# Kernel tuning notes

Measured on AMD Instinct MI355X. Metric: run time of the kernel, lower is better.

Reference implementation:

```python
import jax, jax.numpy as jnp
import numpy as np
import math

B, S, D, H, DK = 2, 4096, 512, 8, 64

def setup_inputs() -> dict:
    key = jax.random.key(0)
    ks = jax.random.split(key, 11)
    scale = 1.0 / math.sqrt(D)
    inp = {
        'q': jax.random.normal(ks[0], (B, S, D), jnp.float32),
        'k': jax.random.normal(ks[1], (B, S, D), jnp.float32),
        'v': jax.random.normal(ks[2], (B, S, D), jnp.float32),
        # causal mask: True = masked (as consumed by masked_fill)
        'mask': jnp.triu(jnp.ones((S, S), jnp.bool_), k=1)[None, None, :, :],
        'wq': jax.random.normal(ks[3], (D, D), jnp.float32) * scale,
        'bq': jnp.zeros((D,), jnp.float32),
        'wk': jax.random.normal(ks[4], (D, D), jnp.float32) * scale,
        'bk': jnp.zeros((D,), jnp.float32),
        'wv': jax.random.normal(ks[5], (D, D), jnp.float32) * scale,
        'bv': jnp.zeros((D,), jnp.float32),
        'wo': jax.random.normal(ks[6], (D, D), jnp.float32) * scale,
        'bo': jnp.zeros((D,), jnp.float32),
    }
    return inp

def reference(q, k, v, mask, wq, bq, wk, bk, wv, bv, wo, bo):
    # torch nn.Linear: y = x @ W^T + b
    def proj(x, w, b):
        return x @ w.T + b
    def heads(x):  # [B,S,D] -> [B,H,S,DK]
        return x.reshape(B, S, H, DK).transpose(0, 2, 1, 3)
    qh = heads(proj(q, wq, bq))
    kh = heads(proj(k, wk, bk))
    vh = heads(proj(v, wv, bv))
    scores = jnp.einsum('bhqd,bhkd->bhqk', qh, kh) / math.sqrt(DK)
    # NOTE: faithful to source, masked positions are filled with -1e-09 (not -inf)
    scores = jnp.where(mask, jnp.float32(-1e-09), scores)
    attn = jax.nn.softmax(scores, axis=-1)
    x = jnp.einsum('bhqk,bhkd->bhqd', attn, vh)
    x = x.transpose(0, 2, 1, 3).reshape(B, S, D)
    return proj(x, wo, bo)
```

## Files before the change

### kernel.cpp

```cpp
#include <hip/hip_runtime.h>
#include <math.h>

#define SS 4096
#define DD 512
#define HH 8
#define DKK 64

#define MSUB 4.0f
#define W_MASK 0.0183156393f
#define CST 136

typedef _Float16 half8_t __attribute__((ext_vector_type(8)));
typedef _Float16 half4_t __attribute__((ext_vector_type(4)));
typedef float f32x4 __attribute__((ext_vector_type(4)));
typedef float f32x16 __attribute__((ext_vector_type(16)));

__device__ __forceinline__ f32x4 mfma16(half8_t a, half8_t b, f32x4 c) {
    return __builtin_amdgcn_mfma_f32_16x16x32_f16(a, b, c, 0, 0, 0);
}
__device__ __forceinline__ f32x16 mfma32(half8_t a, half8_t b, f32x16 c) {
    return __builtin_amdgcn_mfma_f32_32x32x16_f16(a, b, c, 0, 0, 0);
}
__device__ __forceinline__ f32x16 zero16() {
    f32x16 z;
#pragma unroll
    for (int i = 0; i < 16; i++) z[i] = 0.f;
    return z;
}
__device__ __forceinline__ void gld_lds16(const _Float16* g, _Float16* l) {
    __builtin_amdgcn_global_load_lds((const __attribute__((address_space(1))) void*)g,
                                     (__attribute__((address_space(3))) void*)l, 16, 0, 0);
}

__global__ __launch_bounds__(256) void cvt_prep(
    const float* __restrict__ q, const float* __restrict__ k, const float* __restrict__ v,
    const float* __restrict__ wq, const float* __restrict__ wk,
    const float* __restrict__ wv, const float* __restrict__ wo,
    _Float16* qf, _Float16* kf, _Float16* vf,
    _Float16* wqf, _Float16* wkf, _Float16* wvf, _Float16* wof)
{
    const float* srcs[7] = {q, k, v, wq, wk, wv, wo};
    _Float16* dsts[7] = {qf, kf, vf, wqf, wkf, wvf, wof};
    const int ns[7] = {4194304, 4194304, 4194304, 262144, 262144, 262144, 262144};
    int t = blockIdx.y;
    size_t i0 = ((size_t)blockIdx.x * 256 + threadIdx.x) * 8;
    if (i0 >= (size_t)ns[t]) return;
    const float* s = srcs[t];
    _Float16* d = dsts[t];
    float4 a = *(const float4*)(s + i0);
    float4 b = *(const float4*)(s + i0 + 4);
    half8_t h = {(_Float16)a.x, (_Float16)a.y, (_Float16)a.z, (_Float16)a.w,
                 (_Float16)b.x, (_Float16)b.y, (_Float16)b.z, (_Float16)b.w};
    *(half8_t*)(d + i0) = h;
}

__global__ __launch_bounds__(256, 3) void gemm_qkv(
    const _Float16* __restrict__ qf, const _Float16* __restrict__ kf,
    const _Float16* __restrict__ vf,
    const _Float16* __restrict__ wqf, const _Float16* __restrict__ wkf,
    const _Float16* __restrict__ wvf,
    const float* __restrict__ bq, const float* __restrict__ bk,
    const float* __restrict__ bv,
    _Float16* __restrict__ Qf, _Float16* __restrict__ Kf,
    _Float16* __restrict__ Vf, _Float16* __restrict__ Vt)
{
    __shared__ __align__(16) _Float16 smem[17408];
    const int z = blockIdx.z;
    const _Float16* A = z == 0 ? qf : (z == 1 ? kf : vf);
    const _Float16* W = z == 0 ? wqf : (z == 1 ? wkf : wvf);
    const float* bias = z == 0 ? bq : (z == 1 ? bk : bv);

    const int tid = threadIdx.x;
    const int w = tid >> 6, lane = tid & 63, q = lane >> 4, cc = lane & 15;
    const int h5 = lane >> 5, l31 = lane & 31;
    const int mtile = blockIdx.x * 128, ntile = blockIdx.y * 128;
    const int mw = (w & 1) * 64, nw = (w >> 1) * 64;
    const int srow = lane >> 3, scol = (lane & 7) * 8;

    f32x4 acc[4][4];
#pragma unroll
    for (int i = 0; i < 4; i++)
#pragma unroll
        for (int j = 0; j < 4; j++) {
            f32x4 zf = {0.f, 0.f, 0.f, 0.f};
            acc[i][j] = zf;
        }

    for (int kt = 0; kt < 512; kt += 64) {
        __syncthreads();
#pragma unroll
        for (int i = 0; i < 4; i++) {
            int r0 = w * 32 + i * 8;
            gld_lds16(A + (size_t)(mtile + r0 + srow) * 512 + kt + scol, &smem[r0 * 64]);
            gld_lds16(W + (size_t)(ntile + r0 + srow) * 512 + kt + scol, &smem[8192 + r0 * 64]);
        }
        __syncthreads();
#pragma unroll
        for (int kh = 0; kh < 2; kh++) {
            half8_t ar[4], br[4];
#pragma unroll
            for (int i = 0; i < 4; i++)
                ar[i] = *(const half8_t*)(&smem[(mw + i * 16 + cc) * 64 + kh * 32 + q * 8]);
#pragma unroll
            for (int j = 0; j < 4; j++)
                br[j] = *(const half8_t*)(&smem[8192 + (nw + j * 16 + cc) * 64 + kh * 32 + q * 8]);
#pragma unroll
            for (int i = 0; i < 4; i++)
#pragma unroll
                for (int j = 0; j < 4; j++)
                    acc[i][j] = mfma16(ar[i], br[j], acc[i][j]);
        }
    }

    const int b = mtile >> 12;
    const int ms = mtile & 4095;

    __syncthreads();
#pragma unroll
    for (int jb = 0; jb < 4; jb++) {
        int nloc = nw + jb * 16 + cc;
        int n = ntile + nloc;
        float bvv = bias[n];
#pragma unroll
        for (int it = 0; it < 4; it++) {
            int mloc = mw + it * 16 + q * 4;
            half4_t pk;
#pragma unroll
            for (int r = 0; r < 4; r++) {
                _Float16 hv = (_Float16)(acc[it][jb][r] + bvv);
                pk[r] = hv;
                smem[(mloc + r) * CST + nloc] = hv;
            }
            if (z == 2) {
                int bh = b * 8 + (n >> 6);
                int dkl = n & 63;
                *(half4_t*)(Vt + ((size_t)bh * 64 + dkl) * SS + ms + mloc) = pk;
            }
        }
    }
    __syncthreads();

    if (z == 0) {
#pragma unroll
        for (int i = 0; i < 8; i++) {
            int e = w * 8 + i;
            int s5 = e >> 3, hh = (e >> 2) & 1, d4 = e & 3;
            int row = s5 * 32 + l31;
            int col = hh * 64 + d4 * 16 + h5 * 8;
            half8_t vv = *(const half8_t*)(&smem[row * CST + col]);
            int bh = b * 8 + (ntile >> 6) + hh;
            size_t base = ((size_t)(bh * 128 + (ms >> 5) + s5) * 4 + d4) * 512;
            *(half8_t*)(Qf + base + lane * 8) = vv;
        }
    } else if (z == 1) {
#pragma unroll
        for (int i = 0; i < 8; i++) {
            int e = w * 8 + i;
            int s6 = e >> 4, s5b = (e >> 3) & 1, hh = (e >> 2) & 1, d4 = e & 3;
            int row = s6 * 64 + s5b * 32 + l31;
            int col = hh * 64 + d4 * 16 + h5 * 8;
            half8_t vv = *(const half8_t*)(&smem[row * CST + col]);
            int bh = b * 8 + (ntile >> 6) + hh;
            size_t base = ((size_t)(bh * 64 + (ms >> 6) + s6) * 8 + s5b * 4 + d4) * 512;
            *(half8_t*)(Kf + base + lane * 8) = vv;
        }
    } else {
#pragma unroll
        for (int i = 0; i < 8; i++) {
            int e = w * 8 + i;
            int s6 = e >> 4, c = (e >> 2) & 3, hh = (e >> 1) & 1, d5 = e & 1;
            int col = hh * 64 + d5 * 32 + l31;
            half8_t vv;
#pragma unroll
            for (int k0 = 0; k0 < 8; k0++) {
                int mrow = s6 * 64 + c * 16 + (k0 & 3) + 4 * h5 + 8 * (k0 >> 2);
                vv[k0] = smem[mrow * CST + col];
            }
            int bh = b * 8 + (ntile >> 6) + hh;
            size_t base = ((size_t)(bh * 64 + (ms >> 6) + s6) * 8 + c * 2 + d5) * 512;
            *(half8_t*)(Vf + base + lane * 8) = vv;
        }
    }
}

__global__ __launch_bounds__(256) void suffix_v(const _Float16* __restrict__ Vt,
                                                _Float16* __restrict__ SufVt)
{
    __shared__ float csum[4][65];
    const int bh = blockIdx.x >> 4;
    const int dk = (blockIdx.x & 15) * 4 + (threadIdx.x >> 6);
    const int dki = threadIdx.x >> 6;
    const int c = threadIdx.x & 63;
    const _Float16* vp = Vt + ((size_t)bh * 64 + dk) * SS + c * 64;

    half8_t v8[8];
    float acc = 0.f;
#pragma unroll
    for (int j = 0; j < 8; j++) {
        v8[j] = *(const half8_t*)(vp + j * 8);
#pragma unroll
        for (int t = 0; t < 8; t++) acc += (float)v8[j][t];
    }
    csum[dki][c] = acc;
    __syncthreads();
    if (threadIdx.x < 4) {
        float a = 0.f;
        for (int c2 = 63; c2 >= 0; c2--) {
            float t2 = csum[threadIdx.x][c2];
            csum[threadIdx.x][c2] = a;
            a += t2;
        }
    }
    __syncthreads();
    float a = csum[dki][c];
    _Float16* op = SufVt + ((size_t)bh * 64 + dk) * SS + c * 64;
#pragma unroll
    for (int j = 7; j >= 0; j--) {
        half8_t o8;
#pragma unroll
        for (int t = 7; t >= 0; t--) {
            o8[t] = (_Float16)a;
            a += (float)v8[j][t];
        }
        *(half8_t*)(op + j * 8) = o8;
    }
}

__device__ __forceinline__ void exp_pack(const f32x16& s, half8_t& pa, half8_t& pb,
                                         float& lsum) {
#pragma unroll
    for (int i = 0; i < 16; i++) {
        float p = __expf(fmaf(s[i], 0.125f, -MSUB));
        lsum += p;
        if (i < 8) pa[i] = (_Float16)p; else pb[i - 8] = (_Float16)p;
    }
}
__device__ __forceinline__ void exp_pack_mask(const f32x16& s, int j0, int mg, int h5,
                                              half8_t& pa, half8_t& pb, float& lsum) {
#pragma unroll
    for (int i = 0; i < 16; i++) {
        int jg = j0 + (i & 3) + 8 * (i >> 2) + 4 * h5;
        float p = __expf(fmaf(s[i], 0.125f, -MSUB));
        if (jg > mg) p = 0.f;
        lsum += p;
        if (i < 8) pa[i] = (_Float16)p; else pb[i - 8] = (_Float16)p;
    }
}

__global__ __launch_bounds__(128) void attn_part(
    const _Float16* __restrict__ Qf, const _Float16* __restrict__ Kf,
    const _Float16* __restrict__ Vf,
    _Float16* __restrict__ Op0, _Float16* __restrict__ Op1,
    float* __restrict__ Lpart)
{
    const int tid = threadIdx.x;
    const int w = tid >> 6, lane = tid & 63;
    const int h5 = lane >> 5, l31 = lane & 31;
    const int bh = blockIdx.x & 15;
    const int qg = 127 - (int)(blockIdx.x >> 4);
    const int qbase = qg * 32;
    const int jdiag = qbase & ~63;
    const int jsd = (qbase >> 5) & 1;
    const int mg = qbase + l31;
    const int nfull = jdiag >> 6;
    const int T2 = (nfull + 1) >> 1;

    const _Float16* qp = Qf + (size_t)(bh * 128 + (qbase >> 5)) * 4 * 512 + lane * 8;
    half8_t qfr[4];
#pragma unroll
    for (int s = 0; s < 4; s++) qfr[s] = *(const half8_t*)(qp + s * 512);

    const _Float16* Kb = Kf + (size_t)bh * 64 * 4096 + lane * 8;
    const _Float16* Vb = Vf + (size_t)bh * 64 * 4096 + lane * 8;

    f32x16 o0 = zero16(), o1 = zero16();
    float lsum = 0.f;

    const int lo = (w == 0) ? 0 : T2;
    const int hi = (w == 0) ? T2 : nfull;
    for (int jblk = lo; jblk < hi; jblk++) {
        const _Float16* kg = Kb + (size_t)jblk * 4096;
        const _Float16* vg = Vb + (size_t)jblk * 4096;
        f32x16 sa = zero16(), sb = zero16();
#pragma unroll
        for (int s = 0; s < 4; s++)
            sa = mfma32(*(const half8_t*)(kg + s * 512), qfr[s], sa);
#pragma unroll
        for (int s = 0; s < 4; s++)
            sb = mfma32(*(const half8_t*)(kg + (4 + s) * 512), qfr[s], sb);
        half8_t p0a, p0b, p1a, p1b;
        exp_pack(sa, p0a, p0b, lsum);
        exp_pack(sb, p1a, p1b, lsum);
        o0 = mfma32(p0a, *(const half8_t*)(vg + 0 * 512), o0);
        o1 = mfma32(p0a, *(const half8_t*)(vg + 1 * 512), o1);
        o0 = mfma32(p0b, *(const half8_t*)(vg + 2 * 512), o0);
        o1 = mfma32(p0b, *(const half8_t*)(vg + 3 * 512), o1);
        o0 = mfma32(p1a, *(const half8_t*)(vg + 4 * 512), o0);
        o1 = mfma32(p1a, *(const half8_t*)(vg + 5 * 512), o1);
        o0 = mfma32(p1b, *(const half8_t*)(vg + 6 * 512), o0);
        o1 = mfma32(p1b, *(const half8_t*)(vg + 7 * 512), o1);
    }

    if (w == 1) {
        const _Float16* kg = Kb + (size_t)nfull * 4096;
        const _Float16* vg = Vb + (size_t)nfull * 4096;
        f32x16 sa = zero16();
#pragma unroll
        for (int s = 0; s < 4; s++)
            sa = mfma32(*(const half8_t*)(kg + s * 512), qfr[s], sa);
        half8_t p0a, p0b;
        if (jsd == 0) exp_pack_mask(sa, jdiag, mg, h5, p0a, p0b, lsum);
        else          exp_pack(sa, p0a, p0b, lsum);
        o0 = mfma32(p0a, *(const half8_t*)(vg + 0 * 512), o0);
        o1 = mfma32(p0a, *(const half8_t*)(vg + 1 * 512), o1);
        o0 = mfma32(p0b, *(const half8_t*)(vg + 2 * 512), o0);
        o1 = mfma32(p0b, *(const half8_t*)(vg + 3 * 512), o1);
        if (jsd == 1) {
            f32x16 sb = zero16();
#pragma unroll
            for (int s = 0; s < 4; s++)
                sb = mfma32(*(const half8_t*)(kg + (4 + s) * 512), qfr[s], sb);
            half8_t p1a, p1b;
            exp_pack_mask(sb, jdiag + 32, mg, h5, p1a, p1b, lsum);
            o0 = mfma32(p1a, *(const half8_t*)(vg + 4 * 512), o0);
            o1 = mfma32(p1a, *(const half8_t*)(vg + 5 * 512), o1);
            o0 = mfma32(p1b, *(const half8_t*)(vg + 6 * 512), o0);
            o1 = mfma32(p1b, *(const half8_t*)(vg + 7 * 512), o1);
        }
    }

    const size_t task = (size_t)bh * 128 + qg;
    _Float16* Opw = (w == 0 ? Op0 : Op1) + task * 2048;
    Lpart[(task * 2 + w) * 64 + lane] = lsum;
#pragma unroll
    for (int r = 0; r < 16; r++) {
        int row = (r & 3) + 8 * (r >> 2) + 4 * h5;
        Opw[row * 64 + l31] = (_Float16)o0[r];
        Opw[row * 64 + 32 + l31] = (_Float16)o1[r];
    }
}

__global__ __launch_bounds__(256) void attn_reduce(
    const _Float16* __restrict__ Op0, const _Float16* __restrict__ Op1,
    const float* __restrict__ Lpart, const _Float16* __restrict__ SufVt,
    _Float16* __restrict__ X)
{
    __shared__ _Float16 sfv[32 * 64];
    __shared__ float linv[32];
    const int t = threadIdx.x;
    const int bh = blockIdx.x & 15;
    const int qg = blockIdx.x >> 4;
    const int qbase = qg * 32;
    const size_t task = (size_t)bh * 128 + qg;

#pragma unroll
    for (int i = 0; i < 8; i++) {
        int dk = i * 8 + (t >> 5);
        int sl = t & 31;
        sfv[sl * 64 + dk] = SufVt[((size_t)bh * 64 + dk) * SS + qbase + sl];
    }
    if (t < 32) {
        const float* lp = Lpart + task * 128;
        float l = lp[t] + lp[t + 32] + lp[64 + t] + lp[64 + t + 32];
        linv[t] = 1.f / (l + (float)(SS - 1 - qbase - t) * W_MASK);
    }
    __syncthreads();

    const int b = bh >> 3, hh = bh & 7;
    const int dk = t & 63;
    const int r0 = t >> 6;
    const _Float16* oa = Op0 + task * 2048;
    const _Float16* ob = Op1 + task * 2048;
#pragma unroll
    for (int i = 0; i < 8; i++) {
        int r = r0 + 4 * i;
        float o = (float)oa[r * 64 + dk] + (float)ob[r * 64 + dk];
        float val = (o + W_MASK * (float)sfv[r * 64 + dk]) * linv[r];
        int s = qbase + r;
        X[((size_t)b * SS + s) * DD + hh * 64 + dk] = (_Float16)val;
    }
}

__global__ __launch_bounds__(256, 4) void gemm_out(
    const _Float16* __restrict__ A, const _Float16* __restrict__ W,
    const float* __restrict__ bias, float* __restrict__ Cout)
{
    __shared__ __align__(16) _Float16 smem[12288];
    const int tid = threadIdx.x;
    const int w = tid >> 6, lane = tid & 63, q = lane >> 4, cc = lane & 15;
    const int mtile = blockIdx.x * 128, ntile = blockIdx.y * 64;
    const int mw = (w & 1) * 64, nw = (w >> 1) * 32;
    const int srow = lane >> 3, scol = (lane & 7) * 8;

    f32x4 acc[4][2];
#pragma unroll
    for (int i = 0; i < 4; i++)
#pragma unroll
        for (int j = 0; j < 2; j++) {
            f32x4 zf = {0.f, 0.f, 0.f, 0.f};
            acc[i][j] = zf;
        }

    for (int kt = 0; kt < 512; kt += 64) {
        __syncthreads();
#pragma unroll
        for (int i = 0; i < 4; i++) {
            int r0 = w * 32 + i * 8;
            gld_lds16(A + (size_t)(mtile + r0 + srow) * 512 + kt + scol, &smem[r0 * 64]);
        }
#pragma unroll
        for (int i = 0; i < 2; i++) {
            int r0 = w * 16 + i * 8;
            gld_lds16(W + (size_t)(ntile + r0 + srow) * 512 + kt + scol, &smem[8192 + r0 * 64]);
        }
        __syncthreads();
#pragma unroll
        for (int kh = 0; kh < 2; kh++) {
            half8_t ar[4], br[2];
#pragma unroll
            for (int i = 0; i < 4; i++)
                ar[i] = *(const half8_t*)(&smem[(mw + i * 16 + cc) * 64 + kh * 32 + q * 8]);
#pragma unroll
            for (int j = 0; j < 2; j++)
                br[j] = *(const half8_t*)(&smem[8192 + (nw + j * 16 + cc) * 64 + kh * 32 + q * 8]);
#pragma unroll
            for (int i = 0; i < 4; i++)
#pragma unroll
                for (int j = 0; j < 2; j++)
                    acc[i][j] = mfma16(ar[i], br[j], acc[i][j]);
        }
    }

#pragma unroll
    for (int j = 0; j < 2; j++) {
        int coln = ntile + nw + j * 16 + cc;
        float bvv = bias[coln];
#pragma unroll
        for (int i = 0; i < 4; i++) {
            int m0 = mtile + mw + i * 16 + q * 4;
#pragma unroll
            for (int r = 0; r < 4; r++)
                Cout[(size_t)(m0 + r) * 512 + coln] = acc[i][j][r] + bvv;
        }
    }
}

extern "C" void kernel_launch(void* const* d_in, const int* in_sizes, int n_in,
                              void* d_out, int out_size, void* d_ws, size_t ws_size,
                              hipStream_t stream) {
    const float* q  = (const float*)d_in[0];
    const float* k  = (const float*)d_in[1];
    const float* v  = (const float*)d_in[2];
    const float* wq = (const float*)d_in[4];
    const float* bq = (const float*)d_in[5];
    const float* wk = (const float*)d_in[6];
    const float* bk = (const float*)d_in[7];
    const float* wv = (const float*)d_in[8];
    const float* bv = (const float*)d_in[9];
    const float* wo = (const float*)d_in[10];
    const float* bo = (const float*)d_in[11];
    float* out = (float*)d_out;

    char* ws = (char*)d_ws;
    const size_t MB = (size_t)1024 * 1024;
    _Float16* qf  = (_Float16*)(ws);
    _Float16* kf  = (_Float16*)(ws + 8 * MB);
    _Float16* vf  = (_Float16*)(ws + 16 * MB);
    _Float16* wqf = (_Float16*)(ws + 24 * MB);
    _Float16* wkf = (_Float16*)(ws + 24 * MB + 512 * 1024);
    _Float16* wvf = (_Float16*)(ws + 25 * MB);
    _Float16* wof = (_Float16*)(ws + 25 * MB + 512 * 1024);
    _Float16* Qfr = (_Float16*)(ws + 26 * MB);
    _Float16* Kfr = (_Float16*)(ws + 34 * MB);
    _Float16* Vfr = (_Float16*)(ws + 42 * MB);
    _Float16* Vt  = (_Float16*)(ws + 50 * MB);
    float*    Lp  = (float*)(ws + 58 * MB);
    _Float16* SufVt = qf;
    _Float16* Xa    = kf;
    _Float16* Op0   = vf;
    _Float16* Op1   = Vt;

    hipLaunchKernelGGL(cvt_prep, dim3(2048, 7), dim3(256), 0, stream,
                       q, k, v, wq, wk, wv, wo, qf, kf, vf, wqf, wkf, wvf, wof);
    hipLaunchKernelGGL(gemm_qkv, dim3(64, 4, 3), dim3(256), 0, stream,
                       qf, kf, vf, wqf, wkf, wvf, bq, bk, bv, Qfr, Kfr, Vfr, Vt);
    hipLaunchKernelGGL(suffix_v, dim3(256), dim3(256), 0, stream, Vt, SufVt);
    hipLaunchKernelGGL(attn_part, dim3(2048), dim3(128), 0, stream,
                       Qfr, Kfr, Vfr, Op0, Op1, Lp);
    hipLaunchKernelGGL(attn_reduce, dim3(2048), dim3(256), 0, stream,
                       Op0, Op1, Lp, SufVt, Xa);
    hipLaunchKernelGGL(gemm_out, dim3(64, 8), dim3(256), 0, stream, Xa, wof, bo, out);
}
```

Before: 314.9 us.

## Share K/V tiles in LDS across 256-query blocks with balanced split-KV tasks

The attention-partial kernel now processes 256 query rows per 4-wave block. K/V tiles are staged through double-buffered LDS with asynchronous global-to-LDS loads, so all waves reuse each tile instead of each wave reading K/V straight from global memory. Work is split into 30 precomputed chunks per head, balanced over the causal triangle, and each chunk writes a partial output and row sums that the reduce kernel combines. This cuts redundant K/V traffic and the number of tiny blocks, at the cost of more barriers, lookup tables, and a variable-length reduction.

```diff
diff --git a/kernel.cpp b/kernel.cpp
--- a/kernel.cpp
+++ b/kernel.cpp
@@ -247,137 +247,190 @@
     }
 }
 
-__global__ __launch_bounds__(128) void attn_part(
+__global__ __launch_bounds__(256, 2) void attn_part(
     const _Float16* __restrict__ Qf, const _Float16* __restrict__ Kf,
     const _Float16* __restrict__ Vf,
-    _Float16* __restrict__ Op0, _Float16* __restrict__ Op1,
-    float* __restrict__ Lpart)
+    _Float16* __restrict__ Opart, float* __restrict__ Lp)
 {
+    static const int t_qb[30] = {15,15,15,14,14,14,13,13,13,12,12,12,11,11,
+                                 10,10,9,9,8,8,7,7,6,6,5,4,3,2,1,0};
+    static const int t_c0[30] = {0,22,43, 0,20,40, 0,19,38, 0,18,35, 0,24,
+                                 0,22, 0,20, 0,18, 0,16, 0,14, 0, 0, 0, 0, 0, 0};
+    static const int t_nt[30] = {22,21,21,20,20,20,19,19,18,18,17,17,24,24,
+                                 22,22,20,20,18,18,16,16,14,14,24,20,16,12,8,4};
+
+    __shared__ __align__(16) _Float16 lds[16384];
     const int tid = threadIdx.x;
     const int w = tid >> 6, lane = tid & 63;
     const int h5 = lane >> 5, l31 = lane & 31;
     const int bh = blockIdx.x & 15;
-    const int qg = 127 - (int)(blockIdx.x >> 4);
-    const int qbase = qg * 32;
-    const int jdiag = qbase & ~63;
-    const int jsd = (qbase >> 5) & 1;
-    const int mg = qbase + l31;
-    const int nfull = jdiag >> 6;
-    const int T2 = (nfull + 1) >> 1;
-
-    const _Float16* qp = Qf + (size_t)(bh * 128 + (qbase >> 5)) * 4 * 512 + lane * 8;
-    half8_t qfr[4];
-#pragma unroll
-    for (int s = 0; s < 4; s++) qfr[s] = *(const half8_t*)(qp + s * 512);
-
-    const _Float16* Kb = Kf + (size_t)bh * 64 * 4096 + lane * 8;
-    const _Float16* Vb = Vf + (size_t)bh * 64 * 4096 + lane * 8;
-
-    f32x16 o0 = zero16(), o1 = zero16();
-    float lsum = 0.f;
-
-    const int lo = (w == 0) ? 0 : T2;
-    const int hi = (w == 0) ? T2 : nfull;
-    for (int jblk = lo; jblk < hi; jblk++) {
-        const _Float16* kg = Kb + (size_t)jblk * 4096;
-        const _Float16* vg = Vb + (size_t)jblk * 4096;
-        f32x16 sa = zero16(), sb = zero16();
-#pragma unroll
-        for (int s = 0; s < 4; s++)
-            sa = mfma32(*(const half8_t*)(kg + s * 512), qfr[s], sa);
-#pragma unroll
-        for (int s = 0; s < 4; s++)
-            sb = mfma32(*(const half8_t*)(kg + (4 + s) * 512), qfr[s], sb);
-        half8_t p0a, p0b, p1a, p1b;
-        exp_pack(sa, p0a, p0b, lsum);
-        exp_pack(sb, p1a, p1b, lsum);
-        o0 = mfma32(p0a, *(const half8_t*)(vg + 0 * 512), o0);
-        o1 = mfma32(p0a, *(const half8_t*)(vg + 1 * 512), o1);
-        o0 = mfma32(p0b, *(const half8_t*)(vg + 2 * 512), o0);
-        o1 = mfma32(p0b, *(const half8_t*)(vg + 3 * 512), o1);
-        o0 = mfma32(p1a, *(const half8_t*)(vg + 4 * 512), o0);
-        o1 = mfma32(p1a, *(const half8_t*)(vg + 5 * 512), o1);
-        o0 = mfma32(p1b, *(const half8_t*)(vg + 6 * 512), o0);
-        o1 = mfma32(p1b, *(const half8_t*)(vg + 7 * 512), o1);
-    }
-
-    if (w == 1) {
-        const _Float16* kg = Kb + (size_t)nfull * 4096;
-        const _Float16* vg = Vb + (size_t)nfull * 4096;
-        f32x16 sa = zero16();
-#pragma unroll
-        for (int s = 0; s < 4; s++)
-            sa = mfma32(*(const half8_t*)(kg + s * 512), qfr[s], sa);
-        half8_t p0a, p0b;
-        if (jsd == 0) exp_pack_mask(sa, jdiag, mg, h5, p0a, p0b, lsum);
-        else          exp_pack(sa, p0a, p0b, lsum);
-        o0 = mfma32(p0a, *(const half8_t*)(vg + 0 * 512), o0);
-        o1 = mfma32(p0a, *(const half8_t*)(vg + 1 * 512), o1);
-        o0 = mfma32(p0b, *(const half8_t*)(vg + 2 * 512), o0);
-        o1 = mfma32(p0b, *(const half8_t*)(vg + 3 * 512), o1);
-        if (jsd == 1) {
-            f32x16 sb = zero16();
-#pragma unroll
-            for (int s = 0; s < 4; s++)
-                sb = mfma32(*(const half8_t*)(kg + (4 + s) * 512), qfr[s], sb);
-            half8_t p1a, p1b;
-            exp_pack_mask(sb, jdiag + 32, mg, h5, p1a, p1b, lsum);
-            o0 = mfma32(p1a, *(const half8_t*)(vg + 4 * 512), o0);
-            o1 = mfma32(p1a, *(const half8_t*)(vg + 5 * 512), o1);
-            o0 = mfma32(p1b, *(const half8_t*)(vg + 6 * 512), o0);
-            o1 = mfma32(p1b, *(const half8_t*)(vg + 7 * 512), o1);
-        }
-    }
-
-    const size_t task = (size_t)bh * 128 + qg;
-    _Float16* Opw = (w == 0 ? Op0 : Op1) + task * 2048;
-    Lpart[(task * 2 + w) * 64 + lane] = lsum;
+    const int tix = blockIdx.x >> 4;
+    const int qb = t_qb[tix], c0 = t_c0[tix], NT = t_nt[tix];
+    const int qbaseA = qb * 256 + w * 64;
+    const int tdw = qb * 4 + w;
+    const int mgA = qbaseA + l31, mgB = qbaseA + 32 + l31;
+    const int qgA = qb * 8 + w * 2;
+
+    const _Float16* qpA = Qf + ((size_t)(bh * 128 + qgA)) * 2048 + lane * 8;
+    half8_t qA[4], qB[4];
+#pragma unroll
+    for (int s = 0; s < 4; s++) {
+        qA[s] = *(const half8_t*)(qpA + s * 512);
+        qB[s] = *(const half8_t*)(qpA + 2048 + s * 512);
+    }
+
+    const _Float16* Kb = Kf + (size_t)bh * 262144 + lane * 8;
+    const _Float16* Vb = Vf + (size_t)bh * 262144 + lane * 8;
+
+    f32x16 oA0 = zero16(), oA1 = zero16(), oB0 = zero16(), oB1 = zero16();
+    float lsA = 0.f, lsB = 0.f;
+
+    {
+        const _Float16* kg = Kb + (size_t)c0 * 4096;
+        const _Float16* vg = Vb + (size_t)c0 * 4096;
+        gld_lds16(kg + (2 * w) * 512,     &lds[(2 * w) * 512]);
+        gld_lds16(kg + (2 * w + 1) * 512, &lds[(2 * w + 1) * 512]);
+        gld_lds16(vg + (2 * w) * 512,     &lds[4096 + (2 * w) * 512]);
+        gld_lds16(vg + (2 * w + 1) * 512, &lds[4096 + (2 * w + 1) * 512]);
+    }
+
+    for (int t = 0; t < NT; t++) {
+        const int p = (t & 1) * 8192;
+        __syncthreads();
+        if (t + 1 < NT) {
+            const int p2 = 8192 - p;
+            const _Float16* kg = Kb + (size_t)(c0 + t + 1) * 4096;
+            const _Float16* vg = Vb + (size_t)(c0 + t + 1) * 4096;
+            gld_lds16(kg + (2 * w) * 512,     &lds[p2 + (2 * w) * 512]);
+            gld_lds16(kg + (2 * w + 1) * 512, &lds[p2 + (2 * w + 1) * 512]);
+            gld_lds16(vg + (2 * w) * 512,     &lds[p2 + 4096 + (2 * w) * 512]);
+            gld_lds16(vg + (2 * w + 1) * 512, &lds[p2 + 4096 + (2 * w + 1) * 512]);
+        }
+        const int jblk = c0 + t;
+        if (jblk <= tdw) {
+            const bool dg = (jblk == tdw);
+            const _Float16* Lk = &lds[p];
+            const _Float16* Lv = &lds[p + 4096];
+            half8_t pa, pb;
+            {
+                f32x16 s0 = zero16();
+#pragma unroll
+                for (int s = 0; s < 4; s++)
+                    s0 = mfma32(*(const half8_t*)(Lk + s * 512 + lane * 8), qA[s], s0);
+                if (dg) exp_pack_mask(s0, jblk * 64, mgA, h5, pa, pb, lsA);
+                else    exp_pack(s0, pa, pb, lsA);
+                oA0 = mfma32(pa, *(const half8_t*)(Lv + 0 * 512 + lane * 8), oA0);
+                oA1 = mfma32(pa, *(const half8_t*)(Lv + 1 * 512 + lane * 8), oA1);
+                oA0 = mfma32(pb, *(const half8_t*)(Lv + 2 * 512 + lane * 8), oA0);
+                oA1 = mfma32(pb, *(const half8_t*)(Lv + 3 * 512 + lane * 8), oA1);
+                if (!dg) {
+                    f32x16 s1 = zero16();
+#pragma unroll
+                    for (int s = 0; s < 4; s++)
+                        s1 = mfma32(*(const half8_t*)(Lk + (4 + s) * 512 + lane * 8), qA[s], s1);
+                    exp_pack(s1, pa, pb, lsA);
+                    oA0 = mfma32(pa, *(const half8_t*)(Lv + 4 * 512 + lane * 8), oA0);
+                    oA1 = mfma32(pa, *(const half8_t*)(Lv + 5 * 512 + lane * 8), oA1);
+                    oA0 = mfma32(pb, *(const half8_t*)(Lv + 6 * 512 + lane * 8), oA0);
+                    oA1 = mfma32(pb, *(const half8_t*)(Lv + 7 * 512 + lane * 8), oA1);
+                }
+            }
+            {
+                f32x16 s2 = zero16();
+#pragma unroll
+                for (int s = 0; s < 4; s++)
+                    s2 = mfma32(*(const half8_t*)(Lk + s * 512 + lane * 8), qB[s], s2);
+                exp_pack(s2, pa, pb, lsB);
+                oB0 = mfma32(pa, *(const half8_t*)(Lv + 0 * 512 + lane * 8), oB0);
+                oB1 = mfma32(pa, *(const half8_t*)(Lv + 1 * 512 + lane * 8), oB1);
+                oB0 = mfma32(pb, *(const half8_t*)(Lv + 2 * 512 + lane * 8), oB0);
+                oB1 = mfma32(pb, *(const half8_t*)(Lv + 3 * 512 + lane * 8), oB1);
+                f32x16 s3 = zero16();
+#pragma unroll
+                for (int s = 0; s < 4; s++)
+                    s3 = mfma32(*(const half8_t*)(Lk + (4 + s) * 512 + lane * 8), qB[s], s3);
+                if (dg) exp_pack_mask(s3, jblk * 64 + 32, mgB, h5, pa, pb, lsB);
+                else    exp_pack(s3, pa, pb, lsB);
+                oB0 = mfma32(pa, *(const half8_t*)(Lv + 4 * 512 + lane * 8), oB0);
+                oB1 = mfma32(pa, *(const half8_t*)(Lv + 5 * 512 + lane * 8), oB1);
+                oB0 = mfma32(pb, *(const half8_t*)(Lv + 6 * 512 + lane * 8), oB0);
+                oB1 = mfma32(pb, *(const half8_t*)(Lv + 7 * 512 + lane * 8), oB1);
+            }
+        }
+    }
+    __syncthreads();
+
+    lsA += __shfl_xor(lsA, 32);
+    lsB += __shfl_xor(lsB, 32);
+    const size_t task = (size_t)bh * 30 + tix;
+    if (h5 == 0) {
+        Lp[task * 256 + w * 64 + l31] = lsA;
+        Lp[task * 256 + w * 64 + 32 + l31] = lsB;
+    }
+
 #pragma unroll
     for (int r = 0; r < 16; r++) {
         int row = (r & 3) + 8 * (r >> 2) + 4 * h5;
-        Opw[row * 64 + l31] = (_Float16)o0[r];
-        Opw[row * 64 + 32 + l31] = (_Float16)o1[r];
-    }
+        lds[(w * 64 + row) * 64 + l31]            = (_Float16)oA0[r];
+        lds[(w * 64 + row) * 64 + 32 + l31]       = (_Float16)oA1[r];
+        lds[(w * 64 + 32 + row) * 64 + l31]       = (_Float16)oB0[r];
+        lds[(w * 64 + 32 + row) * 64 + 32 + l31]  = (_Float16)oB1[r];
+    }
+    __syncthreads();
+    _Float16* Op = Opart + task * 16384;
+#pragma unroll
+    for (int i = 0; i < 8; i++)
+        *(half8_t*)(Op + i * 2048 + tid * 8) = *(const half8_t*)(&lds[i * 2048 + tid * 8]);
 }
 
 __global__ __launch_bounds__(256) void attn_reduce(
-    const _Float16* __restrict__ Op0, const _Float16* __restrict__ Op1,
-    const float* __restrict__ Lpart, const _Float16* __restrict__ SufVt,
-    _Float16* __restrict__ X)
+    const _Float16* __restrict__ Opart, const float* __restrict__ Lp,
+    const _Float16* __restrict__ SufVt, _Float16* __restrict__ X)
 {
-    __shared__ _Float16 sfv[32 * 64];
-    __shared__ float linv[32];
+    static const int r_n[16]  = {1,1,1,1,1,1,2,2,2,2,2,2,3,3,3,3};
+    static const int r_f0[16] = {29,28,27,26,25,24,22,20,18,16,14,12,9,6,3,0};
+    __shared__ __align__(16) _Float16 sfv[16384];
+    __shared__ float linv[256];
     const int t = threadIdx.x;
-    const int bh = blockIdx.x & 15;
-    const int qg = blockIdx.x >> 4;
-    const int qbase = qg * 32;
-    const size_t task = (size_t)bh * 128 + qg;
-
+    const int bh = blockIdx.x & 15, qb = blockIdx.x >> 4;
+    const int n = r_n[qb];
+    const size_t f0 = (size_t)bh * 30 + r_f0[qb];
+
+    const int dk = t & 63, sblk = t >> 6;
 #pragma unroll
     for (int i = 0; i < 8; i++) {
-        int dk = i * 8 + (t >> 5);
-        int sl = t & 31;
-        sfv[sl * 64 + dk] = SufVt[((size_t)bh * 64 + dk) * SS + qbase + sl];
-    }
-    if (t < 32) {
-        const float* lp = Lpart + task * 128;
-        float l = lp[t] + lp[t + 32] + lp[64 + t] + lp[64 + t + 32];
-        linv[t] = 1.f / (l + (float)(SS - 1 - qbase - t) * W_MASK);
+        half8_t sv = *(const half8_t*)(SufVt + ((size_t)bh * 64 + dk) * SS
+                                       + qb * 256 + sblk * 64 + i * 8);
+#pragma unroll
+        for (int j = 0; j < 8; j++)
+            sfv[(sblk * 64 + i * 8 + j) * 64 + dk] = sv[j];
+    }
+    {
+        float l = 0.f;
+        for (int c = 0; c < n; c++) l += Lp[(f0 + c) * 256 + t];
+        linv[t] = 1.f / (l + (float)(SS - 1 - qb * 256 - t) * W_MASK);
     }
     __syncthreads();
 
     const int b = bh >> 3, hh = bh & 7;
-    const int dk = t & 63;
-    const int r0 = t >> 6;
-    const _Float16* oa = Op0 + task * 2048;
-    const _Float16* ob = Op1 + task * 2048;
 #pragma unroll
     for (int i = 0; i < 8; i++) {
-        int r = r0 + 4 * i;
-        float o = (float)oa[r * 64 + dk] + (float)ob[r * 64 + dk];
-        float val = (o + W_MASK * (float)sfv[r * 64 + dk]) * linv[r];
-        int s = qbase + r;
-        X[((size_t)b * SS + s) * DD + hh * 64 + dk] = (_Float16)val;
+        int e = i * 2048 + t * 8;
+        int row = e >> 6;
+        float iv = linv[row];
+        float acc[8] = {0.f, 0.f, 0.f, 0.f, 0.f, 0.f, 0.f, 0.f};
+        for (int c = 0; c < n; c++) {
+            half8_t o8 = *(const half8_t*)(Opart + (f0 + c) * 16384 + e);
+#pragma unroll
+            for (int j = 0; j < 8; j++) acc[j] += (float)o8[j];
+        }
+        half8_t sv8 = *(const half8_t*)(&sfv[e]);
+        half8_t out8;
+#pragma unroll
+        for (int j = 0; j < 8; j++)
+            out8[j] = (_Float16)((acc[j] + W_MASK * (float)sv8[j]) * iv);
+        int s = qb * 256 + row;
+        *(half8_t*)(X + ((size_t)b * SS + s) * DD + hh * 64 + (e & 63)) = out8;
     }
 }
 
@@ -474,20 +527,19 @@
     _Float16* Kfr = (_Float16*)(ws + 34 * MB);
     _Float16* Vfr = (_Float16*)(ws + 42 * MB);
     _Float16* Vt  = (_Float16*)(ws + 50 * MB);
-    float*    Lp  = (float*)(ws + 58 * MB);
-    _Float16* SufVt = qf;
-    _Float16* Xa    = kf;
-    _Float16* Op0   = vf;
-    _Float16* Op1   = Vt;
+    _Float16* Opart = (_Float16*)(ws);
+    float*    Lp    = (float*)(ws + 15 * MB);
+    _Float16* SufVt = vf;
+    _Float16* Xa    = Vt;
 
     hipLaunchKernelGGL(cvt_prep, dim3(2048, 7), dim3(256), 0, stream,
                        q, k, v, wq, wk, wv, wo, qf, kf, vf, wqf, wkf, wvf, wof);
     hipLaunchKernelGGL(gemm_qkv, dim3(64, 4, 3), dim3(256), 0, stream,
                        qf, kf, vf, wqf, wkf, wvf, bq, bk, bv, Qfr, Kfr, Vfr, Vt);
     hipLaunchKernelGGL(suffix_v, dim3(256), dim3(256), 0, stream, Vt, SufVt);
-    hipLaunchKernelGGL(attn_part, dim3(2048), dim3(128), 0, stream,
-                       Qfr, Kfr, Vfr, Op0, Op1, Lp);
-    hipLaunchKernelGGL(attn_reduce, dim3(2048), dim3(256), 0, stream,
-                       Op0, Op1, Lp, SufVt, Xa);
+    hipLaunchKernelGGL(attn_part, dim3(480), dim3(256), 0, stream,
+                       Qfr, Kfr, Vfr, Opart, Lp);
+    hipLaunchKernelGGL(attn_reduce, dim3(256), dim3(256), 0, stream,
+                       Opart, Lp, SufVt, Xa);
     hipLaunchKernelGGL(gemm_out, dim3(64, 8), dim3(256), 0, stream, Xa, wof, bo, out);
 }
```

Measured after the change: 255.9 us. 18.7% less time.
